# Performance work log

Hardware: AMD Instinct MI355X
Metric: run time of the kernel (lower is better)

Reference implementation:

```python
import jax, jax.numpy as jnp
import numpy as np

B, PLEN, D = 32, 1024, 256


def setup_inputs() -> dict:
    key = jax.random.key(0)
    ks = jax.random.split(key, 8)
    u = lambda k, shape: jax.random.uniform(k, shape, jnp.float32, -0.05, 0.05)
    return {
        "P": jax.random.normal(ks[0], (B, PLEN, D), jnp.float32),
        "w_itr_att": u(ks[1], (3 * D,)),
        "w1": u(ks[2], (2 * D, D)),
        "w2": u(ks[3], (2 * D, D)),
        "w3": u(ks[4], (2 * D, D)),
        "b1": u(ks[5], (D,)),
        "b2": u(ks[6], (D,)),
        "b3": u(ks[7], (D,)),
    }


def reference(P, w_itr_att, w1, w2, w3, b1, b2, b3):
    d = P.shape[-1]
    # alpha(a,b) = w_itr_att . [a ; b ; a*b]; split w into the three d-chunks
    wa, wb, wc = w_itr_att[:d], w_itr_att[d:2 * d], w_itr_att[2 * d:]
    # pairwise score A[b,i,j] = wa.P_i + wb.P_j + wc.(P_i * P_j)
    sa = P @ wa                                   # (b, p)
    sb = P @ wb                                   # (b, p)
    A = sa[:, :, None] + sb[:, None, :] + jnp.einsum('bid,bjd->bij', P * wc, P)
    itr_attn = jnp.einsum('bij,bjd->bid', jax.nn.softmax(A, axis=2), P)
    cat = jnp.concatenate([P, itr_attn], axis=-1)  # (b, p, 2d)
    z = jnp.tanh(cat @ w1 + b1)
    r = jax.nn.sigmoid(cat @ w2 + b2)
    f = jax.nn.sigmoid(cat @ w3 + b3)
    return r * P + f * z
```

## Files before the change

kernel.cpp:

```cpp
#include <hip/hip_runtime.h>
#include <hip/hip_bf16.h>

typedef unsigned short u16;
typedef unsigned int   u32;

using bf16x8 = __attribute__((ext_vector_type(8))) short;
using f32x4  = __attribute__((ext_vector_type(4))) float;

#define NB 32
#define NP 1024
#define ND 256

__device__ __forceinline__ u16 f2bf(float x){
  u32 u = __float_as_uint(x);
  u += 0x7FFFu + ((u >> 16) & 1u);
  return (u16)(u >> 16);
}

__device__ __forceinline__ float bf2f(u16 x){
  return __uint_as_float((u32)x << 16);
}

__device__ __forceinline__ void glds16(const void* g, void* l){
  __builtin_amdgcn_global_load_lds((const __attribute__((address_space(1))) void*)g,
                                   (__attribute__((address_space(3))) void*)l, 16, 0, 0);
}

__global__ void prep_rows(const float* __restrict__ P, const float* __restrict__ wi,
                          u16* __restrict__ Pbf, float* __restrict__ sbv){
  const int row  = blockIdx.x * 4 + (threadIdx.x >> 6);
  const int lane = threadIdx.x & 63;
  const float4 p  = *(const float4*)(P  + (size_t)row * ND + lane * 4);
  const float4 wb = *(const float4*)(wi + ND + lane * 4);
  ushort4 pb;
  pb.x = f2bf(p.x); pb.y = f2bf(p.y); pb.z = f2bf(p.z); pb.w = f2bf(p.w);
  *(ushort4*)(Pbf + (size_t)row * ND + lane * 4) = pb;
  float s = p.x*wb.x + p.y*wb.y + p.z*wb.z + p.w*wb.w;
  #pragma unroll
  for (int m = 1; m < 64; m <<= 1) s += __shfl_xor(s, m, 64);
  if (lane == 0) sbv[row] = s;
}

__global__ void prep_w(const float* __restrict__ w1, const float* __restrict__ w2,
                       const float* __restrict__ w3, u16* __restrict__ Wp){
  const int t = blockIdx.x;
  const float* w = (t < 16) ? w1 : ((t < 32) ? w2 : w3);
  const int tid = threadIdx.x;
  #pragma unroll
  for (int j = 0; j < 4; ++j){
    int item = tid + 256 * j;
    int c = item >> 6, lane = item & 63;
    int ncol = ((t & 15) << 4) + (lane & 15);
    int k0 = 32 * c + 8 * (lane >> 4);
    u16 tmp[8];
    #pragma unroll
    for (int e = 0; e < 8; ++e) tmp[e] = f2bf(w[(size_t)(k0 + e) * 256 + ncol]);
    *(uint4*)(Wp + ((size_t)(t * 16 + c) * 64 + lane) * 8) = *(uint4*)tmp;
  }
}

__global__ void transpose_p(const u16* __restrict__ Pbf, u16* __restrict__ PbfT){
  const int b = blockIdx.z, jt = blockIdx.x, dt = blockIdx.y;
  __shared__ u16 T[64][72];
  const int tid = threadIdx.x;
  #pragma unroll
  for (int it = 0; it < 2; ++it){
    int cc = tid + 256 * it;
    int j = cc >> 3, c8 = cc & 7;
    uint4 v = *(const uint4*)(Pbf + ((size_t)b * NP + jt * 64 + j) * ND + dt * 64 + c8 * 8);
    *(uint4*)&T[j][c8 * 8] = v;
  }
  __syncthreads();
  #pragma unroll
  for (int it = 0; it < 2; ++it){
    int cc = tid + 256 * it;
    int d = cc >> 3, c8 = cc & 7;
    u16 tmp[8];
    #pragma unroll
    for (int k = 0; k < 8; ++k) tmp[k] = T[c8 * 8 + k][d];
    *(uint4*)(PbfT + ((size_t)b * ND + dt * 64 + d) * NP + jt * 64 + c8 * 8) = *(uint4*)tmp;
  }
}

__launch_bounds__(256, 2)
__global__ void attn_kernel(const float* __restrict__ P, const float* __restrict__ wi,
                            const u16* __restrict__ Pbf, const u16* __restrict__ PbfT,
                            const float* __restrict__ sbv, u16* __restrict__ attnb){
  const int p    = blockIdx.x;
  const int bid  = ((p & 7) << 6) | (p >> 3);
  const int b    = bid >> 4;
  const int q0   = (bid & 15) << 6;
  const int tid  = threadIdx.x;
  const int wave = tid >> 6, lane = tid & 63, lo = lane & 15, hi = lane >> 4;

  __shared__ __align__(16) u16 KtA[64 * 256];
  __shared__ __align__(16) u16 VtA[256 * 64];
  __shared__ __align__(16) u16 Sp[4][16][72];
  char* KtB = (char*)KtA;
  char* VtB = (char*)VtA;

  bf16x8 qf[8];
  {
    const int qrow = q0 + wave * 16 + lo;
    const float* prow = P  + ((size_t)b * NP + qrow) * ND;
    const float* wcp  = wi + 512;
    #pragma unroll
    for (int c = 0; c < 8; ++c){
      const int d0 = 32 * c + 8 * hi;
      float4 a  = *(const float4*)(prow + d0);
      float4 a2 = *(const float4*)(prow + d0 + 4);
      float4 wa  = *(const float4*)(wcp + d0);
      float4 wa2 = *(const float4*)(wcp + d0 + 4);
      bf16x8 q;
      q[0]=(short)f2bf(a.x*wa.x);  q[1]=(short)f2bf(a.y*wa.y);
      q[2]=(short)f2bf(a.z*wa.z);  q[3]=(short)f2bf(a.w*wa.w);
      q[4]=(short)f2bf(a2.x*wa2.x); q[5]=(short)f2bf(a2.y*wa2.y);
      q[6]=(short)f2bf(a2.z*wa2.z); q[7]=(short)f2bf(a2.w*wa2.w);
      qf[c] = q;
    }
  }

  f32x4 of[16];
  #pragma unroll
  for (int t = 0; t < 16; ++t) of[t] = (f32x4){0.f,0.f,0.f,0.f};
  float mx[4] = {-1e30f,-1e30f,-1e30f,-1e30f};
  float ls[4] = {0.f,0.f,0.f,0.f};

  const u16* kslab = Pbf  + (size_t)b * NP * ND;
  const u16* vslab = PbfT + (size_t)b * ND * NP;

  auto stageK = [&](int kt){
    const int kbase = kt * 64;
    #pragma unroll
    for (int it = 0; it < 8; ++it){
      int off = it * 4096 + tid * 16;
      int j   = off >> 9;
      int ck  = ((off >> 4) & 31) ^ (j & 7);
      glds16((const char*)(kslab + (size_t)(kbase + j) * ND + ck * 8), KtB + off);
    }
  };
  auto stageV = [&](int kt){
    const int kbase = kt * 64;
    #pragma unroll
    for (int it = 0; it < 8; ++it){
      int off = it * 4096 + tid * 16;
      int d   = off >> 7;
      int kc  = ((off >> 4) & 7) ^ (d & 7);
      glds16((const char*)(vslab + (size_t)d * NP + kbase + kc * 8), VtB + off);
    }
  };

  float sbc[4], sbn[4];
  stageK(0);
  stageV(0);
  #pragma unroll
  for (int nt = 0; nt < 4; ++nt) sbc[nt] = sbv[(size_t)b * NP + nt * 16 + lo];
  __syncthreads();

  for (int kt = 0; kt < 16; ++kt){
    f32x4 s[4];
    #pragma unroll
    for (int nt = 0; nt < 4; ++nt){
      f32x4 acc = (f32x4){0.f,0.f,0.f,0.f};
      #pragma unroll
      for (int c = 0; c < 8; ++c){
        int j  = nt * 16 + lo;
        int ad = j * 512 + (((4 * c + hi) ^ (j & 7)) << 4);
        bf16x8 kf = *(const bf16x8*)(KtB + ad);
        acc = __builtin_amdgcn_mfma_f32_16x16x32_bf16(qf[c], kf, acc, 0, 0, 0);
      }
      s[nt] = acc;
      float sv = sbc[nt];
      #pragma unroll
      for (int r = 0; r < 4; ++r) s[nt][r] += sv;
    }

    __syncthreads();
    if (kt < 15) stageK(kt + 1);

    float md = -1e30f;
    #pragma unroll
    for (int nt = 0; nt < 4; ++nt)
      #pragma unroll
      for (int r = 0; r < 4; ++r) md = fmaxf(md, s[nt][r] - mx[r]);
    if (!__all(md <= 8.f)){
      float scale[4];
      #pragma unroll
      for (int r = 0; r < 4; ++r){
        float v = fmaxf(fmaxf(s[0][r], s[1][r]), fmaxf(s[2][r], s[3][r]));
        v = fmaxf(v, __shfl_xor(v, 1, 64));
        v = fmaxf(v, __shfl_xor(v, 2, 64));
        v = fmaxf(v, __shfl_xor(v, 4, 64));
        v = fmaxf(v, __shfl_xor(v, 8, 64));
        float mnew = fmaxf(mx[r], v);
        scale[r] = __expf(mx[r] - mnew);
        mx[r] = mnew;
        ls[r] *= scale[r];
      }
      #pragma unroll
      for (int t = 0; t < 16; ++t)
        #pragma unroll
        for (int r = 0; r < 4; ++r) of[t][r] *= scale[r];
    }
    #pragma unroll
    for (int nt = 0; nt < 4; ++nt)
      #pragma unroll
      for (int r = 0; r < 4; ++r){
        float pv = __expf(s[nt][r] - mx[r]);
        ls[r] += pv;
        Sp[wave][4 * hi + r][16 * nt + lo] = f2bf(pv);
      }

    #pragma unroll
    for (int kk = 0; kk < 2; ++kk){
      bf16x8 pa = *(const bf16x8*)&Sp[wave][lo][32 * kk + 8 * hi];
      #pragma unroll
      for (int t = 0; t < 16; ++t){
        int d  = 16 * t + lo;
        int ad = d * 128 + (((4 * kk + hi) ^ (d & 7)) << 4);
        bf16x8 vb = *(const bf16x8*)(VtB + ad);
        of[t] = __builtin_amdgcn_mfma_f32_16x16x32_bf16(pa, vb, of[t], 0, 0, 0);
      }
    }

    __syncthreads();
    if (kt < 15){
      stageV(kt + 1);
      #pragma unroll
      for (int nt = 0; nt < 4; ++nt)
        sbn[nt] = sbv[(size_t)b * NP + (kt + 1) * 64 + nt * 16 + lo];
      sbc[0] = sbn[0]; sbc[1] = sbn[1]; sbc[2] = sbn[2]; sbc[3] = sbn[3];
    }
  }

  #pragma unroll
  for (int r = 0; r < 4; ++r){
    ls[r] += __shfl_xor(ls[r], 1, 64);
    ls[r] += __shfl_xor(ls[r], 2, 64);
    ls[r] += __shfl_xor(ls[r], 4, 64);
    ls[r] += __shfl_xor(ls[r], 8, 64);
  }
  const int qrow = q0 + wave * 16;
  #pragma unroll
  for (int t = 0; t < 16; ++t){
    #pragma unroll
    for (int r = 0; r < 4; ++r){
      float o = of[t][r] / ls[r];
      attnb[((size_t)b * NP + qrow + 4 * hi + r) * ND + 16 * t + lo] = f2bf(o);
    }
  }
}

__launch_bounds__(256, 2)
__global__ void mlp_kernel(const u16* __restrict__ Pbf, const u16* __restrict__ attnb,
                           const u16* __restrict__ Wp,
                           const float* __restrict__ b1, const float* __restrict__ b2,
                           const float* __restrict__ b3, float* __restrict__ out){
  const int p    = blockIdx.x;
  const int swz  = ((p & 7) << 7) | (p >> 3);
  const int mt   = swz >> 2, cg = swz & 3;
  const int tid  = threadIdx.x;
  const int wave = tid >> 6, lane = tid & 63, lo = lane & 15, hi = lane >> 4;
  const int tq   = 4 * cg + wave;
  const int m0   = mt * 128;

  __shared__ __align__(16) u16 Ab[2][128 * 64];

  f32x4 acc[3][8];
  #pragma unroll
  for (int e = 0; e < 3; ++e)
    #pragma unroll
    for (int m = 0; m < 8; ++m) acc[e][m] = (f32x4){0.f,0.f,0.f,0.f};

  auto stage = [&](int s, int buf){
    const u16* xs = (s < 4) ? (Pbf   + (size_t)m0 * ND + s * 64)
                            : (attnb + (size_t)m0 * ND + (s - 4) * 64);
    char* dst = (char*)Ab[buf];
    #pragma unroll
    for (int it = 0; it < 4; ++it){
      int off = it * 4096 + wave * 1024 + lane * 16;
      int row = off >> 7;
      int cl  = (off & 127) ^ ((row & 7) << 4);
      glds16((const char*)(xs + (size_t)row * ND) + cl, dst + it * 4096 + wave * 1024);
    }
  };

  stage(0, 0);
  __syncthreads();

  for (int s = 0; s < 8; ++s){
    if (s < 7) stage(s + 1, (s + 1) & 1);
    const char* ab = (const char*)Ab[s & 1];
    #pragma unroll
    for (int cc = 0; cc < 2; ++cc){
      const int c = 2 * s + cc;
      bf16x8 wf[3];
      #pragma unroll
      for (int e = 0; e < 3; ++e)
        wf[e] = *(const bf16x8*)(Wp + ((size_t)((tq + 16 * e) * 16 + c) * 64 + lane) * 8);
      #pragma unroll
      for (int m = 0; m < 8; ++m){
        int row = 16 * m + lo;
        bf16x8 af = *(const bf16x8*)(ab + row * 128 + ((64 * cc + 16 * hi) ^ ((row & 7) << 4)));
        #pragma unroll
        for (int e = 0; e < 3; ++e)
          acc[e][m] = __builtin_amdgcn_mfma_f32_16x16x32_bf16(af, wf[e], acc[e][m], 0, 0, 0);
      }
    }
    __syncthreads();
  }

  const int d = 16 * tq + lo;
  const float bb1 = b1[d], bb2 = b2[d], bb3 = b3[d];
  #pragma unroll
  for (int m = 0; m < 8; ++m){
    #pragma unroll
    for (int r = 0; r < 4; ++r){
      const int row = m0 + 16 * m + 4 * hi + r;
      float y1 = acc[0][m][r] + bb1;
      float y2 = acc[1][m][r] + bb2;
      float y3 = acc[2][m][r] + bb3;
      float pv = bf2f(Pbf[(size_t)row * ND + d]);
      float e2 = __expf(2.f * y1);
      float z  = (e2 - 1.f) / (e2 + 1.f);
      float rr = 1.f / (1.f + __expf(-y2));
      float ff = 1.f / (1.f + __expf(-y3));
      out[(size_t)row * ND + d] = rr * pv + ff * z;
    }
  }
}

extern "C" void kernel_launch(void* const* d_in, const int* in_sizes, int n_in,
                              void* d_out, int out_size, void* d_ws, size_t ws_size,
                              hipStream_t stream){
  const float* P  = (const float*)d_in[0];
  const float* wi = (const float*)d_in[1];
  const float* w1 = (const float*)d_in[2];
  const float* w2 = (const float*)d_in[3];
  const float* w3 = (const float*)d_in[4];
  const float* b1 = (const float*)d_in[5];
  const float* b2 = (const float*)d_in[6];
  const float* b3 = (const float*)d_in[7];
  float* out = (float*)d_out;

  char* ws = (char*)d_ws;
  u16*   Pbf   = (u16*)  (ws);
  u16*   PbfT  = (u16*)  (ws + (16u << 20));
  u16*   attnb = (u16*)  (ws + (32u << 20));
  u16*   Wp    = (u16*)  (ws + (48u << 20));
  float* sbv   = (float*)(ws + (49u << 20));

  prep_rows<<<8192, 256, 0, stream>>>(P, wi, Pbf, sbv);
  prep_w<<<48, 256, 0, stream>>>(w1, w2, w3, Wp);
  transpose_p<<<dim3(16, 4, 32), 256, 0, stream>>>(Pbf, PbfT);
  attn_kernel<<<512, 256, 0, stream>>>(P, wi, Pbf, PbfT, sbv, attnb);
  mlp_kernel<<<1024, 256, 0, stream>>>(Pbf, attnb, Wp, b1, b2, b3, out);
}
```

Baseline: 117.3 us.

## Compute transposed scores to keep softmax probabilities in registers for PV MFMA

Swaps the MFMA operands in the QK product so each lane holds scores for one query row across four keys. That layout feeds the PV product directly through 16x16x16 bf16 MFMAs, removing the shared-memory round trip for the probability tile. Row max and sum now reduce across lanes with shuffles, and the key bias is loaded as a float4 per tile. The cost is twice as many, smaller PV MFMAs, plus 8-byte V reads from LDS.

```diff
diff --git a/kernel.cpp b/kernel.cpp
--- a/kernel.cpp
+++ b/kernel.cpp
@@ -5,6 +5,7 @@
 typedef unsigned int   u32;
 
 using bf16x8 = __attribute__((ext_vector_type(8))) short;
+using bf16x4 = __attribute__((ext_vector_type(4))) short;
 using f32x4  = __attribute__((ext_vector_type(4))) float;
 
 #define NB 32
@@ -25,6 +26,18 @@
   __builtin_amdgcn_global_load_lds((const __attribute__((address_space(1))) void*)g,
                                    (__attribute__((address_space(3))) void*)l, 16, 0, 0);
 }
+
+#if __has_builtin(__builtin_amdgcn_mfma_f32_16x16x16bf16_1k)
+__device__ __forceinline__ f32x4 mfma16(bf16x4 a, bf16x4 b, f32x4 c){
+  return __builtin_amdgcn_mfma_f32_16x16x16bf16_1k(a, b, c, 0, 0, 0);
+}
+#else
+__device__ __forceinline__ f32x4 mfma16(bf16x4 a, bf16x4 b, f32x4 c){
+  bf16x8 a8 = {a[0], a[1], a[2], a[3], 0, 0, 0, 0};
+  bf16x8 b8 = {b[0], b[1], b[2], b[3], 0, 0, 0, 0};
+  return __builtin_amdgcn_mfma_f32_16x16x32_bf16(a8, b8, c, 0, 0, 0);
+}
+#endif
 
 __global__ void prep_rows(const float* __restrict__ P, const float* __restrict__ wi,
                           u16* __restrict__ Pbf, float* __restrict__ sbv){
@@ -95,7 +108,6 @@
 
   __shared__ __align__(16) u16 KtA[64 * 256];
   __shared__ __align__(16) u16 VtA[256 * 64];
-  __shared__ __align__(16) u16 Sp[4][16][72];
   char* KtB = (char*)KtA;
   char* VtB = (char*)VtA;
 
@@ -123,8 +135,8 @@
   f32x4 of[16];
   #pragma unroll
   for (int t = 0; t < 16; ++t) of[t] = (f32x4){0.f,0.f,0.f,0.f};
-  float mx[4] = {-1e30f,-1e30f,-1e30f,-1e30f};
-  float ls[4] = {0.f,0.f,0.f,0.f};
+  float mx = -1e30f;
+  float ls = 0.f;
 
   const u16* kslab = Pbf  + (size_t)b * NP * ND;
   const u16* vslab = PbfT + (size_t)b * ND * NP;
@@ -150,14 +162,13 @@
     }
   };
 
-  float sbc[4], sbn[4];
   stageK(0);
   stageV(0);
-  #pragma unroll
-  for (int nt = 0; nt < 4; ++nt) sbc[nt] = sbv[(size_t)b * NP + nt * 16 + lo];
   __syncthreads();
 
   for (int kt = 0; kt < 16; ++kt){
+    const int kbase = kt * 64;
+
     f32x4 s[4];
     #pragma unroll
     for (int nt = 0; nt < 4; ++nt){
@@ -167,85 +178,81 @@
         int j  = nt * 16 + lo;
         int ad = j * 512 + (((4 * c + hi) ^ (j & 7)) << 4);
         bf16x8 kf = *(const bf16x8*)(KtB + ad);
-        acc = __builtin_amdgcn_mfma_f32_16x16x32_bf16(qf[c], kf, acc, 0, 0, 0);
+        acc = __builtin_amdgcn_mfma_f32_16x16x32_bf16(kf, qf[c], acc, 0, 0, 0);
       }
       s[nt] = acc;
-      float sv = sbc[nt];
-      #pragma unroll
-      for (int r = 0; r < 4; ++r) s[nt][r] += sv;
-    }
-
+    }
     __syncthreads();
     if (kt < 15) stageK(kt + 1);
 
-    float md = -1e30f;
+    #pragma unroll
+    for (int nt = 0; nt < 4; ++nt){
+      float4 sq = *(const float4*)(sbv + (size_t)b * NP + kbase + 16 * nt + 4 * hi);
+      s[nt][0] += sq.x; s[nt][1] += sq.y; s[nt][2] += sq.z; s[nt][3] += sq.w;
+    }
+
+    float vmax = s[0][0];
     #pragma unroll
     for (int nt = 0; nt < 4; ++nt)
       #pragma unroll
-      for (int r = 0; r < 4; ++r) md = fmaxf(md, s[nt][r] - mx[r]);
-    if (!__all(md <= 8.f)){
-      float scale[4];
-      #pragma unroll
-      for (int r = 0; r < 4; ++r){
-        float v = fmaxf(fmaxf(s[0][r], s[1][r]), fmaxf(s[2][r], s[3][r]));
-        v = fmaxf(v, __shfl_xor(v, 1, 64));
-        v = fmaxf(v, __shfl_xor(v, 2, 64));
-        v = fmaxf(v, __shfl_xor(v, 4, 64));
-        v = fmaxf(v, __shfl_xor(v, 8, 64));
-        float mnew = fmaxf(mx[r], v);
-        scale[r] = __expf(mx[r] - mnew);
-        mx[r] = mnew;
-        ls[r] *= scale[r];
-      }
+      for (int r = 0; r < 4; ++r) vmax = fmaxf(vmax, s[nt][r]);
+    if (!__all(vmax - mx <= 8.f)){
+      float v = fmaxf(vmax, __shfl_xor(vmax, 16, 64));
+      v = fmaxf(v, __shfl_xor(v, 32, 64));
+      float mnew = fmaxf(mx, v);
+      float sc = __expf(mx - mnew);
+      mx = mnew; ls *= sc;
+      float scr[4];
+      #pragma unroll
+      for (int r = 0; r < 4; ++r) scr[r] = __shfl(sc, 4 * hi + r, 64);
       #pragma unroll
       for (int t = 0; t < 16; ++t)
         #pragma unroll
-        for (int r = 0; r < 4; ++r) of[t][r] *= scale[r];
-    }
-    #pragma unroll
-    for (int nt = 0; nt < 4; ++nt)
-      #pragma unroll
-      for (int r = 0; r < 4; ++r){
-        float pv = __expf(s[nt][r] - mx[r]);
-        ls[r] += pv;
-        Sp[wave][4 * hi + r][16 * nt + lo] = f2bf(pv);
-      }
-
-    #pragma unroll
-    for (int kk = 0; kk < 2; ++kk){
-      bf16x8 pa = *(const bf16x8*)&Sp[wave][lo][32 * kk + 8 * hi];
+        for (int r = 0; r < 4; ++r) of[t][r] *= scr[r];
+    }
+    bf16x4 pa[4];
+    #pragma unroll
+    for (int nt = 0; nt < 4; ++nt){
+      float e0 = __expf(s[nt][0] - mx);
+      float e1 = __expf(s[nt][1] - mx);
+      float e2 = __expf(s[nt][2] - mx);
+      float e3 = __expf(s[nt][3] - mx);
+      ls += (e0 + e1) + (e2 + e3);
+      bf16x4 w;
+      w[0] = (short)f2bf(e0); w[1] = (short)f2bf(e1);
+      w[2] = (short)f2bf(e2); w[3] = (short)f2bf(e3);
+      pa[nt] = w;
+    }
+
+    #pragma unroll
+    for (int nt = 0; nt < 4; ++nt){
+      const int cswz = (2 * nt + (hi >> 1));
+      const int sub  = 8 * (hi & 1);
       #pragma unroll
       for (int t = 0; t < 16; ++t){
         int d  = 16 * t + lo;
-        int ad = d * 128 + (((4 * kk + hi) ^ (d & 7)) << 4);
-        bf16x8 vb = *(const bf16x8*)(VtB + ad);
-        of[t] = __builtin_amdgcn_mfma_f32_16x16x32_bf16(pa, vb, of[t], 0, 0, 0);
+        int ad = d * 128 + ((cswz ^ (d & 7)) << 4) + sub;
+        bf16x4 vb = *(const bf16x4*)(VtB + ad);
+        of[t] = mfma16(pa[nt], vb, of[t]);
       }
     }
 
     __syncthreads();
-    if (kt < 15){
-      stageV(kt + 1);
-      #pragma unroll
-      for (int nt = 0; nt < 4; ++nt)
-        sbn[nt] = sbv[(size_t)b * NP + (kt + 1) * 64 + nt * 16 + lo];
-      sbc[0] = sbn[0]; sbc[1] = sbn[1]; sbc[2] = sbn[2]; sbc[3] = sbn[3];
-    }
-  }
-
-  #pragma unroll
-  for (int r = 0; r < 4; ++r){
-    ls[r] += __shfl_xor(ls[r], 1, 64);
-    ls[r] += __shfl_xor(ls[r], 2, 64);
-    ls[r] += __shfl_xor(ls[r], 4, 64);
-    ls[r] += __shfl_xor(ls[r], 8, 64);
-  }
+    if (kt < 15) stageV(kt + 1);
+  }
+
+  float ltot = ls;
+  ltot += __shfl_xor(ltot, 16, 64);
+  ltot += __shfl_xor(ltot, 32, 64);
+  float lr[4];
+  #pragma unroll
+  for (int r = 0; r < 4; ++r) lr[r] = __shfl(ltot, 4 * hi + r, 64);
   const int qrow = q0 + wave * 16;
   #pragma unroll
   for (int t = 0; t < 16; ++t){
     #pragma unroll
     for (int r = 0; r < 4; ++r){
-      float o = of[t][r] / ls[r];
+      float o = of[t][r] / lr[r];
       attnb[((size_t)b * NP + qrow + 4 * hi + r) * ND + 16 * t + lo] = f2bf(o);
     }
   }
```

Measured after the change: 126.5 us. 7.8% more time.
